# Kernel tuning notes

Hardware: AMD Instinct MI355X
Metric: run time of the kernel (lower is better)

Reference implementation:

```python
import jax, jax.numpy as jnp
import numpy as np

D = 768        # embed dim
DEPTH = 12     # num blocks
H = 12         # heads
HD = D // H    # head dim = 64
P = 16         # patch size
IMG = 224
NPATCH = (IMG // P) ** 2   # 196
N = NPATCH + 1             # +cls = 197
MLP = 4 * D                # 3072
NC = 100                   # classes
R = 8                      # lora rank
LORA_SCALE = 16.0 / R      # alpha / r = 2.0
EPS = 1e-6                 # timm LayerNorm eps


def setup_inputs() -> dict:
    key = jax.random.key(0)
    ks = jax.random.split(key, 12)
    def g(k, shape, s=0.02):
        return jax.random.normal(k, shape, dtype=jnp.float32) * s
    f32 = jnp.float32
    return {
        "x": jax.random.normal(ks[0], (32, 3, IMG, IMG), dtype=f32),
        "patch_w": g(ks[1], (D, 3, P, P)),
        "patch_b": jnp.zeros((D,), f32),
        "cls_token": g(ks[2], (1, 1, D)),
        "pos_embed": g(ks[3], (1, N, D)),
        "ln1_g": jnp.ones((DEPTH, D), f32),  "ln1_b": jnp.zeros((DEPTH, D), f32),
        "qkv_w": g(ks[4], (DEPTH, 3 * D, D)), "qkv_b": jnp.zeros((DEPTH, 3 * D), f32),
        "lora_A": g(ks[5], (DEPTH, D, R), 0.1), "lora_B": g(ks[6], (DEPTH, R, 3 * D), 0.1),
        "proj_w": g(ks[7], (DEPTH, D, D)), "proj_b": jnp.zeros((DEPTH, D), f32),
        "ln2_g": jnp.ones((DEPTH, D), f32),  "ln2_b": jnp.zeros((DEPTH, D), f32),
        "fc1_w": g(ks[8], (DEPTH, MLP, D)), "fc1_b": jnp.zeros((DEPTH, MLP), f32),
        "fc2_w": g(ks[9], (DEPTH, D, MLP)), "fc2_b": jnp.zeros((DEPTH, D), f32),
        "norm_g": jnp.ones((D,), f32), "norm_b": jnp.zeros((D,), f32),
        "head_w": g(ks[10], (NC, D)), "head_b": jnp.zeros((NC,), f32),
    }


def _ln(x, g, b):
    m = x.mean(-1, keepdims=True)
    v = ((x - m) ** 2).mean(-1, keepdims=True)
    return (x - m) * jax.lax.rsqrt(v + EPS) * g + b


def reference(x, patch_w, patch_b, cls_token, pos_embed,
              ln1_g, ln1_b, qkv_w, qkv_b, lora_A, lora_B, proj_w, proj_b,
              ln2_g, ln2_b, fc1_w, fc1_b, fc2_w, fc2_b,
              norm_g, norm_b, head_w, head_b):
    B = x.shape[0]
    # patch embed: non-overlapping PxP conv == unfold + linear
    xp = x.reshape(B, 3, IMG // P, P, IMG // P, P).transpose(0, 2, 4, 1, 3, 5)
    xp = xp.reshape(B, NPATCH, 3 * P * P)              # [B, 196, 768]
    t = xp @ patch_w.reshape(D, -1).T + patch_b        # [B, 196, D]
    t = jnp.concatenate([jnp.broadcast_to(cls_token, (B, 1, D)), t], axis=1)
    t = t + pos_embed                                   # [B, N, D]

    scale = HD ** -0.5
    for i in range(DEPTH):
        h = _ln(t, ln1_g[i], ln1_b[i])
        # frozen qkv GEMM + LoRA low-rank branch (dropout = identity at eval)
        qkv = h @ qkv_w[i].T + qkv_b[i] + ((h @ lora_A[i]) @ lora_B[i]) * LORA_SCALE
        qkv = qkv.reshape(B, N, 3, H, HD).transpose(2, 0, 3, 1, 4)  # [3, B, H, N, HD]
        q, k, v = qkv[0], qkv[1], qkv[2]
        attn = jax.nn.softmax(jnp.einsum('bhqd,bhkd->bhqk', q, k) * scale, axis=-1)
        o = jnp.einsum('bhqk,bhkd->bhqd', attn, v).transpose(0, 2, 1, 3).reshape(B, N, D)
        t = t + o @ proj_w[i].T + proj_b[i]
        h2 = _ln(t, ln2_g[i], ln2_b[i])
        t = t + jax.nn.gelu(h2 @ fc1_w[i].T + fc1_b[i], approximate=False) @ fc2_w[i].T + fc2_b[i]

    t = _ln(t, norm_g, norm_b)
    return t[:, 0] @ head_w.T + head_b  # cls-token pool -> head [B, NC]
```

## Files before the change

kernel.cpp:

```cpp
#include <hip/hip_runtime.h>

#define TOK  6304
#define MPAD 6400
#define NH   12
#define HD   64
#define BHD  384
#define NPD  256
#define QKVD 2304

typedef float  f32x4  __attribute__((ext_vector_type(4)));
typedef __bf16 bf16x8 __attribute__((ext_vector_type(8)));

__device__ __forceinline__ unsigned short f2bf(float f) {
  unsigned u = __float_as_uint(f);
  return (unsigned short)((u + 0x7fffu + ((u >> 16) & 1u)) >> 16);
}
__device__ __forceinline__ float bf2f(unsigned short h) {
  return __uint_as_float(((unsigned)h) << 16);
}

__device__ __forceinline__ void gl2lds16(void* g, void* l) {
  __builtin_amdgcn_global_load_lds((__attribute__((address_space(1))) void*)g,
                                   (__attribute__((address_space(3))) void*)l, 16, 0, 0);
}

template<int BM, int BN, int MT, int NT, int WC>
__device__ __forceinline__ void gemm_core(const unsigned short* A, int lda,
                                          const unsigned short* B, int ldb,
                                          int K, int bm, int bn,
                                          unsigned short* lds,
                                          f32x4 (&acc)[MT][NT]) {
  const int tid  = threadIdx.x;
  const int wave = tid >> 6, lane = tid & 63;
  const int wr = wave / WC, wc = wave % WC;
  const int lh = lane >> 4, lm = lane & 15;
  unsigned short* ldsA = lds;
  unsigned short* ldsB = lds + BM * 32;
  constexpr int AIT = BM / 64, BIT = BN / 64;
  for (int k0 = 0; k0 < K; k0 += 32) {
    #pragma unroll
    for (int it = 0; it < AIT; ++it) {
      int idx16 = (wave * AIT + it) * 64 + lane;
      int row = idx16 >> 2, seg = idx16 & 3;
      gl2lds16((void*)(A + (long)(bm + row) * lda + k0 + seg * 8), ldsA + idx16 * 8);
    }
    #pragma unroll
    for (int it = 0; it < BIT; ++it) {
      int idx16 = (wave * BIT + it) * 64 + lane;
      int row = idx16 >> 2, seg = idx16 & 3;
      gl2lds16((void*)(B + (long)(bn + row) * ldb + k0 + seg * 8), ldsB + idx16 * 8);
    }
    __syncthreads();
    bf16x8 af[MT], bfr[NT];
    #pragma unroll
    for (int i = 0; i < MT; ++i)
      af[i] = *(const bf16x8*)(ldsA + (wr * MT * 16 + i * 16 + lm) * 32 + lh * 8);
    #pragma unroll
    for (int j = 0; j < NT; ++j)
      bfr[j] = *(const bf16x8*)(ldsB + (wc * NT * 16 + j * 16 + lm) * 32 + lh * 8);
    #pragma unroll
    for (int i = 0; i < MT; ++i)
      #pragma unroll
      for (int j = 0; j < NT; ++j)
        acc[i][j] = __builtin_amdgcn_mfma_f32_16x16x32_bf16(af[i], bfr[j], acc[i][j], 0, 0, 0);
    __syncthreads();
  }
}


__global__ __launch_bounds__(256) void k_cvt(const float4* __restrict__ s,
                                             ushort4* __restrict__ d, int n4) {
  int stride = gridDim.x * 256;
  for (int i = blockIdx.x * 256 + threadIdx.x; i < n4; i += stride) {
    float4 v = s[i];
    ushort4 o;
    o.x = f2bf(v.x); o.y = f2bf(v.y); o.z = f2bf(v.z); o.w = f2bf(v.w);
    d[i] = o;
  }
}

__global__ __launch_bounds__(256) void k_unfold(const float* __restrict__ x,
                                                unsigned short* __restrict__ xp) {
  int idx = blockIdx.x * 256 + threadIdx.x;
  if (idx >= 32 * 196 * 768) return;
  int f = idx % 768; int rest = idx / 768;
  int p = rest % 196; int b = rest / 196;
  int c = f >> 8, ij = f & 255, i = ij >> 4, j = ij & 15;
  int py = p / 14, px = p % 14;
  xp[idx] = f2bf(x[(((long)b * 3 + c) * 224 + py * 16 + i) * 224 + px * 16 + j]);
}

__global__ __launch_bounds__(256) void k_cls(const float* __restrict__ cls,
                                             const float* __restrict__ pos,
                                             float* __restrict__ t) {
  int i = blockIdx.x * 256 + threadIdx.x;
  int b = i / 768, d = i % 768;
  t[((long)(b * 197)) * 768 + d] = cls[d] + pos[d];
}

__global__ __launch_bounds__(256) void k_ln(const float* __restrict__ t,
                                            const float* __restrict__ gw,
                                            const float* __restrict__ bw,
                                            unsigned short* __restrict__ h) {
  __shared__ float red[4];
  int row = blockIdx.x, tid = threadIdx.x;
  const float* x = t + (long)row * 768;
  float v0 = x[tid], v1 = x[tid + 256], v2 = x[tid + 512];
  float s = v0 + v1 + v2;
  #pragma unroll
  for (int off = 32; off > 0; off >>= 1) s += __shfl_xor(s, off, 64);
  int wave = tid >> 6, lane = tid & 63;
  if (lane == 0) red[wave] = s;
  __syncthreads();
  s = red[0] + red[1] + red[2] + red[3];
  float mean = s * (1.f / 768.f);
  float d0 = v0 - mean, d1 = v1 - mean, d2 = v2 - mean;
  float s2 = d0 * d0 + d1 * d1 + d2 * d2;
  __syncthreads();
  #pragma unroll
  for (int off = 32; off > 0; off >>= 1) s2 += __shfl_xor(s2, off, 64);
  if (lane == 0) red[wave] = s2;
  __syncthreads();
  s2 = red[0] + red[1] + red[2] + red[3];
  float rstd = rsqrtf(s2 * (1.f / 768.f) + 1e-6f);
  unsigned short* hr = h + (long)row * 768;
  hr[tid]       = f2bf(d0 * rstd * gw[tid]       + bw[tid]);
  hr[tid + 256] = f2bf(d1 * rstd * gw[tid + 256] + bw[tid + 256]);
  hr[tid + 512] = f2bf(d2 * rstd * gw[tid + 512] + bw[tid + 512]);
}

__global__ __launch_bounds__(256) void k_lora(const unsigned short* __restrict__ h,
                                              const float* __restrict__ A,
                                              float* __restrict__ hA) {
  int row = blockIdx.x, tid = threadIdx.x;
  float a[8];
  #pragma unroll
  for (int r = 0; r < 8; ++r) a[r] = 0.f;
  const unsigned short* hr = h + (long)row * 768;
  for (int kx = tid; kx < 768; kx += 256) {
    float hv = bf2f(hr[kx]);
    const float* Ar = A + kx * 8;
    #pragma unroll
    for (int r = 0; r < 8; ++r) a[r] += hv * Ar[r];
  }
  #pragma unroll
  for (int r = 0; r < 8; ++r) {
    #pragma unroll
    for (int off = 32; off > 0; off >>= 1) a[r] += __shfl_xor(a[r], off, 64);
  }
  __shared__ float red[32];
  int wave = tid >> 6, lane = tid & 63;
  if (lane == 0) {
    #pragma unroll
    for (int r = 0; r < 8; ++r) red[wave * 8 + r] = a[r];
  }
  __syncthreads();
  if (tid < 8) hA[(long)row * 8 + tid] = red[tid] + red[8 + tid] + red[16 + tid] + red[24 + tid];
}

__global__ __launch_bounds__(256) void k_head(const float* __restrict__ t,
                                              const float* __restrict__ ng,
                                              const float* __restrict__ nb,
                                              const float* __restrict__ hw,
                                              const float* __restrict__ hb,
                                              float* __restrict__ out) {
  __shared__ float xs[768];
  __shared__ float red[4];
  int b = blockIdx.x, tid = threadIdx.x;
  const float* x = t + ((long)(b * 197)) * 768;
  float v0 = x[tid], v1 = x[tid + 256], v2 = x[tid + 512];
  float s = v0 + v1 + v2;
  #pragma unroll
  for (int off = 32; off > 0; off >>= 1) s += __shfl_xor(s, off, 64);
  int wave = tid >> 6, lane = tid & 63;
  if (lane == 0) red[wave] = s;
  __syncthreads();
  s = red[0] + red[1] + red[2] + red[3];
  float mean = s * (1.f / 768.f);
  float d0 = v0 - mean, d1 = v1 - mean, d2 = v2 - mean;
  float s2 = d0 * d0 + d1 * d1 + d2 * d2;
  __syncthreads();
  #pragma unroll
  for (int off = 32; off > 0; off >>= 1) s2 += __shfl_xor(s2, off, 64);
  if (lane == 0) red[wave] = s2;
  __syncthreads();
  s2 = red[0] + red[1] + red[2] + red[3];
  float rstd = rsqrtf(s2 * (1.f / 768.f) + 1e-6f);
  xs[tid]       = d0 * rstd * ng[tid]       + nb[tid];
  xs[tid + 256] = d1 * rstd * ng[tid + 256] + nb[tid + 256];
  xs[tid + 512] = d2 * rstd * ng[tid + 512] + nb[tid + 512];
  __syncthreads();
  for (int n = tid; n < 100; n += 256) {
    const float* wr = hw + (long)n * 768;
    float acc = hb[n];
    for (int k2 = 0; k2 < 768; ++k2) acc += xs[k2] * wr[k2];
    out[b * 100 + n] = acc;
  }
}


__global__ __launch_bounds__(256) void k_patch_gemm(
    const unsigned short* __restrict__ xp, const unsigned short* __restrict__ w,
    const float* __restrict__ bias, const float* __restrict__ pos,
    float* __restrict__ t) {
  __shared__ unsigned short lds[(128 + 128) * 32];
  f32x4 acc[4][4] = {};
  int bm = blockIdx.x * 128, bn = blockIdx.y * 128;
  gemm_core<128, 128, 4, 4, 2>(xp, 768, w, 768, 768, bm, bn, lds, acc);
  const int wave = threadIdx.x >> 6, lane = threadIdx.x & 63;
  const int wr = wave >> 1, wc = wave & 1, lh = lane >> 4, lm = lane & 15;
  #pragma unroll
  for (int i = 0; i < 4; ++i)
  #pragma unroll
  for (int r = 0; r < 4; ++r) {
    int m = bm + wr * 64 + i * 16 + lh * 4 + r;
    int b = m / 196, p = m % 196;
    long trow = ((long)(b * 197 + 1 + p)) * 768;
    #pragma unroll
    for (int j = 0; j < 4; ++j) {
      int n = bn + wc * 64 + j * 16 + lm;
      t[trow + n] = acc[i][j][r] + bias[n] + pos[(1 + p) * 768 + n];
    }
  }
}

__global__ __launch_bounds__(256) void k_qkv(
    const unsigned short* __restrict__ h, const unsigned short* __restrict__ w,
    const float* __restrict__ bias, const float* __restrict__ hA,
    const float* __restrict__ loraB,
    unsigned short* __restrict__ q, unsigned short* __restrict__ kk,
    unsigned short* __restrict__ vT) {
  __shared__ unsigned short lds[(128 + 128) * 32];
  f32x4 acc[4][4] = {};
  int bm = blockIdx.x * 128, bn = blockIdx.y * 128;
  gemm_core<128, 128, 4, 4, 2>(h, 768, w, 768, 768, bm, bn, lds, acc);
  const int wave = threadIdx.x >> 6, lane = threadIdx.x & 63;
  const int wr = wave >> 1, wc = wave & 1, lh = lane >> 4, lm = lane & 15;
  #pragma unroll
  for (int i = 0; i < 4; ++i)
  #pragma unroll
  for (int r = 0; r < 4; ++r) {
    int m = bm + wr * 64 + i * 16 + lh * 4 + r;
    if (m >= TOK) continue;
    int b = m / 197, tok = m % 197;
    const float* ha = hA + (long)m * 8;
    #pragma unroll
    for (int j = 0; j < 4; ++j) {
      int n = bn + wc * 64 + j * 16 + lm;
      float lora = 0.f;
      #pragma unroll
      for (int rr = 0; rr < 8; ++rr) lora += ha[rr] * loraB[rr * QKVD + n];
      float v = acc[i][j][r] + bias[n] + 2.0f * lora;
      int which = n / 768;
      int nr = n - which * 768;
      int hh = nr >> 6, dd = nr & 63;
      long base = (long)(b * NH + hh);
      unsigned short bv = f2bf(v);
      if (which == 0)      q [(base * NPD + tok) * HD + dd] = bv;
      else if (which == 1) kk[(base * NPD + tok) * HD + dd] = bv;
      else                 vT[(base * HD + dd) * NPD + tok] = bv;
    }
  }
}

__global__ __launch_bounds__(256) void k_attn_s(
    const unsigned short* __restrict__ q, const unsigned short* __restrict__ kk,
    unsigned short* __restrict__ P) {
  __shared__ unsigned short lds[(128 + 256) * 32];
  f32x4 acc[2][16] = {};
  int bh = blockIdx.y;
  const unsigned short* Q = q  + (long)bh * NPD * HD;
  const unsigned short* K_ = kk + (long)bh * NPD * HD;
  gemm_core<128, 256, 2, 16, 1>(Q, HD, K_, HD, HD, blockIdx.x * 128, 0, lds, acc);
  const int wave = threadIdx.x >> 6, lane = threadIdx.x & 63;
  const int lh = lane >> 4, lm = lane & 15;
  long Pbase = (long)bh * NPD * NPD;
  #pragma unroll
  for (int i = 0; i < 2; ++i) {
    #pragma unroll
    for (int r = 0; r < 4; ++r) {
      float sv[16]; float mx = -3e38f;
      #pragma unroll
      for (int j = 0; j < 16; ++j) {
        float s = acc[i][j][r] * 0.125f;
        if (j * 16 + lm >= 197) s = -3e38f;
        sv[j] = s; mx = fmaxf(mx, s);
      }
      #pragma unroll
      for (int off = 1; off < 16; off <<= 1) mx = fmaxf(mx, __shfl_xor(mx, off, 64));
      float sum = 0.f;
      #pragma unroll
      for (int j = 0; j < 16; ++j) {
        float e = (sv[j] < -1e38f) ? 0.f : __expf(sv[j] - mx);
        sv[j] = e; sum += e;
      }
      #pragma unroll
      for (int off = 1; off < 16; off <<= 1) sum += __shfl_xor(sum, off, 64);
      float inv = 1.f / sum;
      int row = blockIdx.x * 128 + wave * 32 + i * 16 + lh * 4 + r;
      long rowb = Pbase + (long)row * NPD + lm;
      #pragma unroll
      for (int j = 0; j < 16; ++j) P[rowb + j * 16] = f2bf(sv[j] * inv);
    }
  }
}

__global__ __launch_bounds__(256) void k_attn_pv(
    const unsigned short* __restrict__ P, const unsigned short* __restrict__ vT,
    unsigned short* __restrict__ o) {
  __shared__ unsigned short lds[(128 + 64) * 32];
  f32x4 acc[2][4] = {};
  int bh = blockIdx.y;
  int b = bh / NH, hh = bh % NH;
  gemm_core<128, 64, 2, 4, 1>(P + (long)bh * NPD * NPD, NPD,
                              vT + (long)bh * HD * NPD, NPD,
                              NPD, blockIdx.x * 128, 0, lds, acc);
  const int wave = threadIdx.x >> 6, lane = threadIdx.x & 63;
  const int lh = lane >> 4, lm = lane & 15;
  #pragma unroll
  for (int i = 0; i < 2; ++i)
  #pragma unroll
  for (int r = 0; r < 4; ++r) {
    int m = blockIdx.x * 128 + wave * 32 + i * 16 + lh * 4 + r;
    if (m >= 197) continue;
    long ob = ((long)(b * 197 + m)) * 768 + hh * 64;
    #pragma unroll
    for (int j = 0; j < 4; ++j) o[ob + j * 16 + lm] = f2bf(acc[i][j][r]);
  }
}

__global__ __launch_bounds__(256) void k_proj(
    const unsigned short* __restrict__ o, const unsigned short* __restrict__ w,
    const float* __restrict__ bias, float* __restrict__ t) {
  __shared__ unsigned short lds[(128 + 128) * 32];
  f32x4 acc[4][4] = {};
  int bm = blockIdx.x * 128, bn = blockIdx.y * 128;
  gemm_core<128, 128, 4, 4, 2>(o, 768, w, 768, 768, bm, bn, lds, acc);
  const int wave = threadIdx.x >> 6, lane = threadIdx.x & 63;
  const int wr = wave >> 1, wc = wave & 1, lh = lane >> 4, lm = lane & 15;
  #pragma unroll
  for (int i = 0; i < 4; ++i)
  #pragma unroll
  for (int r = 0; r < 4; ++r) {
    int m = bm + wr * 64 + i * 16 + lh * 4 + r;
    if (m >= TOK) continue;
    long trow = (long)m * 768;
    #pragma unroll
    for (int j = 0; j < 4; ++j) {
      int n = bn + wc * 64 + j * 16 + lm;
      t[trow + n] = acc[i][j][r] + bias[n] + t[trow + n];
    }
  }
}

__global__ __launch_bounds__(256) void k_fc1(
    const unsigned short* __restrict__ h, const unsigned short* __restrict__ w,
    const float* __restrict__ bias, unsigned short* __restrict__ g) {
  __shared__ unsigned short lds[(128 + 128) * 32];
  f32x4 acc[4][4] = {};
  int bm = blockIdx.x * 128, bn = blockIdx.y * 128;
  gemm_core<128, 128, 4, 4, 2>(h, 768, w, 768, 768, bm, bn, lds, acc);
  const int wave = threadIdx.x >> 6, lane = threadIdx.x & 63;
  const int wr = wave >> 1, wc = wave & 1, lh = lane >> 4, lm = lane & 15;
  #pragma unroll
  for (int i = 0; i < 4; ++i)
  #pragma unroll
  for (int r = 0; r < 4; ++r) {
    int m = bm + wr * 64 + i * 16 + lh * 4 + r;
    if (m >= TOK) continue;
    long grow = (long)m * 3072;
    #pragma unroll
    for (int j = 0; j < 4; ++j) {
      int n = bn + wc * 64 + j * 16 + lm;
      float u = acc[i][j][r] + bias[n];
      float ge = 0.5f * u * (1.f + erff(u * 0.70710678118654752440f));
      g[grow + n] = f2bf(ge);
    }
  }
}

__global__ __launch_bounds__(256) void k_fc2(
    const unsigned short* __restrict__ g, const unsigned short* __restrict__ w,
    const float* __restrict__ bias, float* __restrict__ t) {
  __shared__ unsigned short lds[(128 + 128) * 32];
  f32x4 acc[4][4] = {};
  int bm = blockIdx.x * 128, bn = blockIdx.y * 128;
  gemm_core<128, 128, 4, 4, 2>(g, 3072, w, 3072, 3072, bm, bn, lds, acc);
  const int wave = threadIdx.x >> 6, lane = threadIdx.x & 63;
  const int wr = wave >> 1, wc = wave & 1, lh = lane >> 4, lm = lane & 15;
  #pragma unroll
  for (int i = 0; i < 4; ++i)
  #pragma unroll
  for (int r = 0; r < 4; ++r) {
    int m = bm + wr * 64 + i * 16 + lh * 4 + r;
    if (m >= TOK) continue;
    long trow = (long)m * 768;
    #pragma unroll
    for (int j = 0; j < 4; ++j) {
      int n = bn + wc * 64 + j * 16 + lm;
      t[trow + n] = acc[i][j][r] + bias[n] + t[trow + n];
    }
  }
}


extern "C" void kernel_launch(void* const* d_in, const int* in_sizes, int n_in,
                              void* d_out, int out_size, void* d_ws, size_t ws_size,
                              hipStream_t stream) {
  const float* x       = (const float*)d_in[0];
  const float* patch_w = (const float*)d_in[1];
  const float* patch_b = (const float*)d_in[2];
  const float* cls_tok = (const float*)d_in[3];
  const float* pos     = (const float*)d_in[4];
  const float* ln1_g   = (const float*)d_in[5];
  const float* ln1_b   = (const float*)d_in[6];
  const float* qkv_w   = (const float*)d_in[7];
  const float* qkv_b   = (const float*)d_in[8];
  const float* lora_A  = (const float*)d_in[9];
  const float* lora_B  = (const float*)d_in[10];
  const float* proj_w  = (const float*)d_in[11];
  const float* proj_b  = (const float*)d_in[12];
  const float* ln2_g   = (const float*)d_in[13];
  const float* ln2_b   = (const float*)d_in[14];
  const float* fc1_w   = (const float*)d_in[15];
  const float* fc1_b   = (const float*)d_in[16];
  const float* fc2_w   = (const float*)d_in[17];
  const float* fc2_b   = (const float*)d_in[18];
  const float* norm_g  = (const float*)d_in[19];
  const float* norm_b  = (const float*)d_in[20];
  const float* head_w  = (const float*)d_in[21];
  const float* head_b  = (const float*)d_in[22];
  float* out = (float*)d_out;
  (void)in_sizes; (void)n_in; (void)out_size;

  char* cur = (char*)d_ws;
  size_t used = 0;
  auto take = [&](size_t bytes) -> char* {
    char* r = cur;
    size_t pad = (bytes + 255) & ~(size_t)255;
    cur += pad; used += pad;
    return r;
  };
  unsigned short* xp  = (unsigned short*)take((size_t)6272 * 768 * 2);
  float*          t   = (float*)take((size_t)MPAD * 768 * 4);
  unsigned short* h   = (unsigned short*)take((size_t)MPAD * 768 * 2);
  float*          hA  = (float*)take((size_t)MPAD * 8 * 4);
  unsigned short* q   = (unsigned short*)take((size_t)BHD * NPD * HD * 2);
  unsigned short* kk  = (unsigned short*)take((size_t)BHD * NPD * HD * 2);
  unsigned short* vT  = (unsigned short*)take((size_t)BHD * NPD * HD * 2);
  unsigned short* P   = (unsigned short*)take((size_t)BHD * NPD * NPD * 2);
  unsigned short* o   = (unsigned short*)take((size_t)MPAD * 768 * 2);
  unsigned short* g   = (unsigned short*)take((size_t)MPAD * 3072 * 2);
  unsigned short* wpatch = (unsigned short*)take((size_t)768 * 768 * 2);

  const size_t EQKV = (size_t)12 * 2304 * 768, EPROJ = (size_t)12 * 768 * 768,
               EFC1 = (size_t)12 * 3072 * 768, EFC2 = (size_t)12 * 768 * 3072;
  size_t fullBytes = (EQKV + EPROJ + EFC1 + EFC2) * 2 + 4 * 256;
  bool full = (ws_size > used) && (ws_size - used >= fullBytes);
  unsigned short *wqkv = 0, *wproj = 0, *wfc1 = 0, *wfc2 = 0, *wbuf = 0;
  if (full) {
    wqkv  = (unsigned short*)take(EQKV * 2);
    wproj = (unsigned short*)take(EPROJ * 2);
    wfc1  = (unsigned short*)take(EFC1 * 2);
    wfc2  = (unsigned short*)take(EFC2 * 2);
  } else {
    wbuf  = (unsigned short*)take((size_t)3072 * 768 * 2);
  }

  auto cvt = [&](const float* src, unsigned short* dst, size_t n) {
    int n4 = (int)(n / 4);
    int grid = (n4 + 255) / 256; if (grid > 4096) grid = 4096;
    k_cvt<<<grid, 256, 0, stream>>>((const float4*)src, (ushort4*)dst, n4);
  };

  cvt(patch_w, wpatch, (size_t)768 * 768);
  if (full) {
    cvt(qkv_w,  wqkv,  EQKV);
    cvt(proj_w, wproj, EPROJ);
    cvt(fc1_w,  wfc1,  EFC1);
    cvt(fc2_w,  wfc2,  EFC2);
  }

  k_unfold<<<(32 * 196 * 768 + 255) / 256, 256, 0, stream>>>(x, xp);
  k_cls<<<(32 * 768) / 256, 256, 0, stream>>>(cls_tok, pos, t);
  k_patch_gemm<<<dim3(49, 6), 256, 0, stream>>>(xp, wpatch, patch_b, pos, t);

  for (int i = 0; i < 12; ++i) {
    k_ln<<<TOK, 256, 0, stream>>>(t, ln1_g + i * 768, ln1_b + i * 768, h);
    k_lora<<<TOK, 256, 0, stream>>>(h, lora_A + (size_t)i * 768 * 8, hA);
    const unsigned short* wq;
    if (full) wq = wqkv + (size_t)i * 2304 * 768;
    else { cvt(qkv_w + (size_t)i * 2304 * 768, wbuf, (size_t)2304 * 768); wq = wbuf; }
    k_qkv<<<dim3(50, 18), 256, 0, stream>>>(h, wq, qkv_b + (size_t)i * 2304,
                                            hA, lora_B + (size_t)i * 8 * 2304, q, kk, vT);
    k_attn_s<<<dim3(2, BHD), 256, 0, stream>>>(q, kk, P);
    k_attn_pv<<<dim3(2, BHD), 256, 0, stream>>>(P, vT, o);
    const unsigned short* wp;
    if (full) wp = wproj + (size_t)i * 768 * 768;
    else { cvt(proj_w + (size_t)i * 768 * 768, wbuf, (size_t)768 * 768); wp = wbuf; }
    k_proj<<<dim3(50, 6), 256, 0, stream>>>(o, wp, proj_b + (size_t)i * 768, t);
    k_ln<<<TOK, 256, 0, stream>>>(t, ln2_g + i * 768, ln2_b + i * 768, h);
    const unsigned short* w1;
    if (full) w1 = wfc1 + (size_t)i * 3072 * 768;
    else { cvt(fc1_w + (size_t)i * 3072 * 768, wbuf, (size_t)3072 * 768); w1 = wbuf; }
    k_fc1<<<dim3(50, 24), 256, 0, stream>>>(h, w1, fc1_b + (size_t)i * 3072, g);
    const unsigned short* w2;
    if (full) w2 = wfc2 + (size_t)i * 768 * 3072;
    else { cvt(fc2_w + (size_t)i * 768 * 3072, wbuf, (size_t)768 * 3072); w2 = wbuf; }
    k_fc2<<<dim3(50, 6), 256, 0, stream>>>(g, w2, fc2_b + (size_t)i * 768, t);
  }

  k_head<<<32, 256, 0, stream>>>(t, norm_g, norm_b, head_w, head_b, out);
}
```

Baseline: 4.500 ms.

## Fuse attention score/softmax with PV via LDS and fold LoRA-A into LayerNorm

The attention score+softmax and PV kernels become one kernel: the normalized probability tile stays in padded LDS instead of going out to a global P buffer and being read back. The LoRA-A projection moves into the first LayerNorm kernel, which removes a launch and a re-read of h. The qkv epilogue also hoists the LoRA-B and bias loads out of the row loop. The price is a larger LDS footprint per block (about 72 KB), which may lower occupancy, and a PV loop with no pipelining.

```diff
diff --git a/kernel.cpp b/kernel.cpp
--- a/kernel.cpp
+++ b/kernel.cpp
@@ -7,6 +7,7 @@
 #define BHD  384
 #define NPD  256
 #define QKVD 2304
+#define PSTR 264
 
 typedef float  f32x4  __attribute__((ext_vector_type(4)));
 typedef __bf16 bf16x8 __attribute__((ext_vector_type(8)));
@@ -101,8 +102,11 @@
 __global__ __launch_bounds__(256) void k_ln(const float* __restrict__ t,
                                             const float* __restrict__ gw,
                                             const float* __restrict__ bw,
-                                            unsigned short* __restrict__ h) {
+                                            unsigned short* __restrict__ h,
+                                            const float* __restrict__ A,
+                                            float* __restrict__ hA) {
   __shared__ float red[4];
+  __shared__ float red8[32];
   int row = blockIdx.x, tid = threadIdx.x;
   const float* x = t + (long)row * 768;
   float v0 = x[tid], v1 = x[tid + 256], v2 = x[tid + 512];
@@ -123,39 +127,32 @@
   __syncthreads();
   s2 = red[0] + red[1] + red[2] + red[3];
   float rstd = rsqrtf(s2 * (1.f / 768.f) + 1e-6f);
+  float n0 = d0 * rstd * gw[tid]       + bw[tid];
+  float n1 = d1 * rstd * gw[tid + 256] + bw[tid + 256];
+  float n2 = d2 * rstd * gw[tid + 512] + bw[tid + 512];
   unsigned short* hr = h + (long)row * 768;
-  hr[tid]       = f2bf(d0 * rstd * gw[tid]       + bw[tid]);
-  hr[tid + 256] = f2bf(d1 * rstd * gw[tid + 256] + bw[tid + 256]);
-  hr[tid + 512] = f2bf(d2 * rstd * gw[tid + 512] + bw[tid + 512]);
-}
-
-__global__ __launch_bounds__(256) void k_lora(const unsigned short* __restrict__ h,
-                                              const float* __restrict__ A,
-                                              float* __restrict__ hA) {
-  int row = blockIdx.x, tid = threadIdx.x;
-  float a[8];
-  #pragma unroll
-  for (int r = 0; r < 8; ++r) a[r] = 0.f;
-  const unsigned short* hr = h + (long)row * 768;
-  for (int kx = tid; kx < 768; kx += 256) {
-    float hv = bf2f(hr[kx]);
-    const float* Ar = A + kx * 8;
-    #pragma unroll
-    for (int r = 0; r < 8; ++r) a[r] += hv * Ar[r];
-  }
-  #pragma unroll
-  for (int r = 0; r < 8; ++r) {
-    #pragma unroll
-    for (int off = 32; off > 0; off >>= 1) a[r] += __shfl_xor(a[r], off, 64);
-  }
-  __shared__ float red[32];
-  int wave = tid >> 6, lane = tid & 63;
-  if (lane == 0) {
-    #pragma unroll
-    for (int r = 0; r < 8; ++r) red[wave * 8 + r] = a[r];
-  }
-  __syncthreads();
-  if (tid < 8) hA[(long)row * 8 + tid] = red[tid] + red[8 + tid] + red[16 + tid] + red[24 + tid];
+  hr[tid]       = f2bf(n0);
+  hr[tid + 256] = f2bf(n1);
+  hr[tid + 512] = f2bf(n2);
+  if (A) {
+    float a[8];
+    const float* A0 = A + (long)tid * 8;
+    const float* A1 = A + (long)(tid + 256) * 8;
+    const float* A2 = A + (long)(tid + 512) * 8;
+    #pragma unroll
+    for (int rr = 0; rr < 8; ++rr) a[rr] = n0 * A0[rr] + n1 * A1[rr] + n2 * A2[rr];
+    #pragma unroll
+    for (int rr = 0; rr < 8; ++rr) {
+      #pragma unroll
+      for (int off = 32; off > 0; off >>= 1) a[rr] += __shfl_xor(a[rr], off, 64);
+    }
+    if (lane == 0) {
+      #pragma unroll
+      for (int rr = 0; rr < 8; ++rr) red8[wave * 8 + rr] = a[rr];
+    }
+    __syncthreads();
+    if (tid < 8) hA[(long)row * 8 + tid] = red8[tid] + red8[8 + tid] + red8[16 + tid] + red8[24 + tid];
+  }
 }
 
 __global__ __launch_bounds__(256) void k_head(const float* __restrict__ t,
@@ -236,6 +233,15 @@
   gemm_core<128, 128, 4, 4, 2>(h, 768, w, 768, 768, bm, bn, lds, acc);
   const int wave = threadIdx.x >> 6, lane = threadIdx.x & 63;
   const int wr = wave >> 1, wc = wave & 1, lh = lane >> 4, lm = lane & 15;
+  float lb[4][8];
+  float bia[4];
+  #pragma unroll
+  for (int j = 0; j < 4; ++j) {
+    int n = bn + wc * 64 + j * 16 + lm;
+    bia[j] = bias[n];
+    #pragma unroll
+    for (int rr = 0; rr < 8; ++rr) lb[j][rr] = loraB[rr * QKVD + n];
+  }
   #pragma unroll
   for (int i = 0; i < 4; ++i)
   #pragma unroll
@@ -244,13 +250,16 @@
     if (m >= TOK) continue;
     int b = m / 197, tok = m % 197;
     const float* ha = hA + (long)m * 8;
+    float hv[8];
+    #pragma unroll
+    for (int rr = 0; rr < 8; ++rr) hv[rr] = ha[rr];
     #pragma unroll
     for (int j = 0; j < 4; ++j) {
       int n = bn + wc * 64 + j * 16 + lm;
       float lora = 0.f;
       #pragma unroll
-      for (int rr = 0; rr < 8; ++rr) lora += ha[rr] * loraB[rr * QKVD + n];
-      float v = acc[i][j][r] + bias[n] + 2.0f * lora;
+      for (int rr = 0; rr < 8; ++rr) lora += hv[rr] * lb[j][rr];
+      float v = acc[i][j][r] + bia[j] + 2.0f * lora;
       int which = n / 768;
       int nr = n - which * 768;
       int hh = nr >> 6, dd = nr & 63;
@@ -263,18 +272,18 @@
   }
 }
 
-__global__ __launch_bounds__(256) void k_attn_s(
+__global__ __launch_bounds__(256) void k_attn(
     const unsigned short* __restrict__ q, const unsigned short* __restrict__ kk,
-    unsigned short* __restrict__ P) {
-  __shared__ unsigned short lds[(128 + 256) * 32];
+    const unsigned short* __restrict__ vT, unsigned short* __restrict__ o) {
+  __shared__ unsigned short lds[128 * PSTR + 64 * 32];
   f32x4 acc[2][16] = {};
   int bh = blockIdx.y;
-  const unsigned short* Q = q  + (long)bh * NPD * HD;
-  const unsigned short* K_ = kk + (long)bh * NPD * HD;
-  gemm_core<128, 256, 2, 16, 1>(Q, HD, K_, HD, HD, blockIdx.x * 128, 0, lds, acc);
-  const int wave = threadIdx.x >> 6, lane = threadIdx.x & 63;
+  int bm = blockIdx.x * 128;
+  gemm_core<128, 256, 2, 16, 1>(q + (long)bh * NPD * HD, HD,
+                                kk + (long)bh * NPD * HD, HD, HD, bm, 0, lds, acc);
+  const int tid = threadIdx.x, wave = tid >> 6, lane = tid & 63;
   const int lh = lane >> 4, lm = lane & 15;
-  long Pbase = (long)bh * NPD * NPD;
+  unsigned short* Plds = lds;
   #pragma unroll
   for (int i = 0; i < 2; ++i) {
     #pragma unroll
@@ -297,35 +306,41 @@
       #pragma unroll
       for (int off = 1; off < 16; off <<= 1) sum += __shfl_xor(sum, off, 64);
       float inv = 1.f / sum;
-      int row = blockIdx.x * 128 + wave * 32 + i * 16 + lh * 4 + r;
-      long rowb = Pbase + (long)row * NPD + lm;
-      #pragma unroll
-      for (int j = 0; j < 16; ++j) P[rowb + j * 16] = f2bf(sv[j] * inv);
-    }
-  }
-}
-
-__global__ __launch_bounds__(256) void k_attn_pv(
-    const unsigned short* __restrict__ P, const unsigned short* __restrict__ vT,
-    unsigned short* __restrict__ o) {
-  __shared__ unsigned short lds[(128 + 64) * 32];
-  f32x4 acc[2][4] = {};
-  int bh = blockIdx.y;
+      int row = wave * 32 + i * 16 + lh * 4 + r;
+      #pragma unroll
+      for (int j = 0; j < 16; ++j) Plds[row * PSTR + j * 16 + lm] = f2bf(sv[j] * inv);
+    }
+  }
+  f32x4 acc2[2][4] = {};
+  const unsigned short* V = vT + (long)bh * HD * NPD;
+  unsigned short* Vst = lds + 128 * PSTR;
+  for (int k0 = 0; k0 < NPD; k0 += 32) {
+    gl2lds16((void*)(V + (long)(tid >> 2) * NPD + k0 + (tid & 3) * 8), Vst + tid * 8);
+    __syncthreads();
+    bf16x8 af[2], bfr[4];
+    #pragma unroll
+    for (int i = 0; i < 2; ++i)
+      af[i] = *(const bf16x8*)(Plds + (wave * 32 + i * 16 + lm) * PSTR + k0 + lh * 8);
+    #pragma unroll
+    for (int j = 0; j < 4; ++j)
+      bfr[j] = *(const bf16x8*)(Vst + (j * 16 + lm) * 32 + lh * 8);
+    #pragma unroll
+    for (int i = 0; i < 2; ++i)
+      #pragma unroll
+      for (int j = 0; j < 4; ++j)
+        acc2[i][j] = __builtin_amdgcn_mfma_f32_16x16x32_bf16(af[i], bfr[j], acc2[i][j], 0, 0, 0);
+    __syncthreads();
+  }
   int b = bh / NH, hh = bh % NH;
-  gemm_core<128, 64, 2, 4, 1>(P + (long)bh * NPD * NPD, NPD,
-                              vT + (long)bh * HD * NPD, NPD,
-                              NPD, blockIdx.x * 128, 0, lds, acc);
-  const int wave = threadIdx.x >> 6, lane = threadIdx.x & 63;
-  const int lh = lane >> 4, lm = lane & 15;
   #pragma unroll
   for (int i = 0; i < 2; ++i)
   #pragma unroll
   for (int r = 0; r < 4; ++r) {
-    int m = blockIdx.x * 128 + wave * 32 + i * 16 + lh * 4 + r;
+    int m = bm + wave * 32 + i * 16 + lh * 4 + r;
     if (m >= 197) continue;
     long ob = ((long)(b * 197 + m)) * 768 + hh * 64;
     #pragma unroll
-    for (int j = 0; j < 4; ++j) o[ob + j * 16 + lm] = f2bf(acc[i][j][r]);
+    for (int j = 0; j < 4; ++j) o[ob + j * 16 + lm] = f2bf(acc2[i][j][r]);
   }
 }
 
@@ -448,7 +463,6 @@
   unsigned short* q   = (unsigned short*)take((size_t)BHD * NPD * HD * 2);
   unsigned short* kk  = (unsigned short*)take((size_t)BHD * NPD * HD * 2);
   unsigned short* vT  = (unsigned short*)take((size_t)BHD * NPD * HD * 2);
-  unsigned short* P   = (unsigned short*)take((size_t)BHD * NPD * NPD * 2);
   unsigned short* o   = (unsigned short*)take((size_t)MPAD * 768 * 2);
   unsigned short* g   = (unsigned short*)take((size_t)MPAD * 3072 * 2);
   unsigned short* wpatch = (unsigned short*)take((size_t)768 * 768 * 2);
@@ -486,20 +500,20 @@
   k_patch_gemm<<<dim3(49, 6), 256, 0, stream>>>(xp, wpatch, patch_b, pos, t);
 
   for (int i = 0; i < 12; ++i) {
-    k_ln<<<TOK, 256, 0, stream>>>(t, ln1_g + i * 768, ln1_b + i * 768, h);
-    k_lora<<<TOK, 256, 0, stream>>>(h, lora_A + (size_t)i * 768 * 8, hA);
+    k_ln<<<TOK, 256, 0, stream>>>(t, ln1_g + i * 768, ln1_b + i * 768, h,
+                                  lora_A + (size_t)i * 768 * 8, hA);
     const unsigned short* wq;
     if (full) wq = wqkv + (size_t)i * 2304 * 768;
     else { cvt(qkv_w + (size_t)i * 2304 * 768, wbuf, (size_t)2304 * 768); wq = wbuf; }
     k_qkv<<<dim3(50, 18), 256, 0, stream>>>(h, wq, qkv_b + (size_t)i * 2304,
                                             hA, lora_B + (size_t)i * 8 * 2304, q, kk, vT);
-    k_attn_s<<<dim3(2, BHD), 256, 0, stream>>>(q, kk, P);
-    k_attn_pv<<<dim3(2, BHD), 256, 0, stream>>>(P, vT, o);
+    k_attn<<<dim3(2, BHD), 256, 0, stream>>>(q, kk, vT, o);
     const unsigned short* wp;
     if (full) wp = wproj + (size_t)i * 768 * 768;
     else { cvt(proj_w + (size_t)i * 768 * 768, wbuf, (size_t)768 * 768); wp = wbuf; }
     k_proj<<<dim3(50, 6), 256, 0, stream>>>(o, wp, proj_b + (size_t)i * 768, t);
-    k_ln<<<TOK, 256, 0, stream>>>(t, ln2_g + i * 768, ln2_b + i * 768, h);
+    k_ln<<<TOK, 256, 0, stream>>>(t, ln2_g + i * 768, ln2_b + i * 768, h,
+                                  (const float*)nullptr, (float*)nullptr);
     const unsigned short* w1;
     if (full) w1 = wfc1 + (size_t)i * 3072 * 768;
     else { cvt(fc1_w + (size_t)i * 3072 * 768, wbuf, (size_t)3072 * 768); w1 = wbuf; }
```

Measured after the change: 4.024 ms. 1.12x faster.
